# Kernel optimization log

Hardware: AMD Instinct MI355X
Metric: run time of the kernel (lower is better)

Reference implementation:

```python
import jax, jax.numpy as jnp
import numpy as np

N_QUBITS = 8
N_LAYERS = 4


def _apply_1q(state, U, q):
    """Apply a 2x2 gate U (shape (2,2) shared, or (B,2,2) per-sample) on qubit q.
    state: (B, 2, 2, ..., 2) with qubit q on axis q+1 (wire 0 = most significant)."""
    a = q + 1
    st = jnp.moveaxis(state, a, -1)
    shp = st.shape
    st = st.reshape(shp[0], -1, 2)  # (B, rest, 2)
    if U.ndim == 3:
        st = jnp.einsum('bij,brj->bri', U, st)
    else:
        st = jnp.einsum('ij,brj->bri', U, st)
    return jnp.moveaxis(st.reshape(shp), -1, a)


def _cnot(state, c, t):
    ac, at = c + 1, t + 1
    s0 = jnp.take(state, 0, axis=ac)
    s1 = jnp.take(state, 1, axis=ac)
    at2 = at - 1 if at > ac else at  # axis shift after removing control axis
    s1 = jnp.flip(s1, axis=at2)      # X on target where control = 1
    return jnp.stack([s0, s1], axis=ac)


def _rx(t):
    c = jnp.cos(t / 2)
    s = jnp.sin(t / 2)
    return jnp.stack([jnp.stack([c + 0j, -1j * s]),
                      jnp.stack([-1j * s, c + 0j])]).astype(jnp.complex64)


def _ry(t):
    c = jnp.cos(t / 2)
    s = jnp.sin(t / 2)
    return jnp.stack([jnp.stack([c, -s]),
                      jnp.stack([s, c])]).astype(jnp.complex64)


def _rz(t):
    return jnp.diag(jnp.stack([jnp.exp(-1j * t / 2),
                               jnp.exp(1j * t / 2)])).astype(jnp.complex64)


def _ry_batched(t):
    # t: (B,) -> (B, 2, 2)
    c = jnp.cos(t / 2)
    s = jnp.sin(t / 2)
    U = jnp.stack([jnp.stack([c, -s], axis=-1),
                   jnp.stack([s, c], axis=-1)], axis=-2)
    return U.astype(jnp.complex64)


def setup_inputs() -> dict:
    key = jax.random.key(0)
    k1, k2 = jax.random.split(key)
    B = 16384
    x = jax.random.normal(k1, (B, N_QUBITS), dtype=jnp.float32)
    weights = jax.random.normal(k2, (N_QUBITS * N_LAYERS * 3,), dtype=jnp.float32) * 0.1
    return {"x": x, "weights": weights}


def reference(x, weights):
    n, L = N_QUBITS, N_LAYERS
    B = x.shape[0]
    state = jnp.zeros((B,) + (2,) * n, dtype=jnp.complex64)
    state = state.at[(slice(None),) + (0,) * n].set(1.0)

    # angle encoding: per-sample RY on each wire
    for q in range(n):
        state = _apply_1q(state, _ry_batched(x[:, q]), q)

    idx = 0
    for _ in range(L):
        for q in range(n):
            state = _apply_1q(state, _rx(weights[idx]), q)
            state = _apply_1q(state, _ry(weights[idx + 1]), q)
            state = _apply_1q(state, _rz(weights[idx + 2]), q)
            idx += 3
        for q in range(n - 1):
            state = _cnot(state, q, q + 1)

    p = jnp.abs(state) ** 2  # (B, 2, ..., 2) float32
    outs = []
    for q in range(n):
        axes = tuple(a for a in range(1, n + 1) if a != q + 1)
        z = p.sum(axis=axes)  # (B, 2)
        outs.append(z[:, 0] - z[:, 1])
    return jnp.stack(outs, axis=-1).astype(jnp.float32)
```

## Files before the change

kernel.cpp:

```cpp
#include <hip/hip_runtime.h>


#define NGATES 32
typedef short s8v __attribute__((ext_vector_type(8)));
typedef float f4v __attribute__((ext_vector_type(4)));

__device__ __forceinline__ unsigned short f2bf(float f) {
    unsigned u = __float_as_uint(f);
    u += 0x7FFFu + ((u >> 16) & 1u);
    return (unsigned short)(u >> 16);
}
__device__ __forceinline__ float xsgn(float f, unsigned m) {
    return __int_as_float(__float_as_int(f) ^ (int)m);
}
template<int M>
__device__ __forceinline__ float shx(float v) {
    return __int_as_float(__builtin_amdgcn_ds_swizzle(__float_as_int(v), (M << 10) | 0x1F));
}

constexpr bool selon(int l, int d) {
    return (l == 0) ? (d == 0) : (((d + l - 1) & (l - 1)) == (l - 1));
}
constexpr int lm_of(int l, int q) {
    int m = 0;
    for (int d = 0; q + d <= 7; ++d)
        if ((l & d) == d) { int qq = q + d; if (qq <= 3) m |= 1 << (3 - qq); }
    return m;
}
constexpr int rm_of(int l, int q) {
    int m = 0;
    for (int d = 0; q + d <= 7; ++d)
        if ((l & d) == d) { int qq = q + d; if (qq >= 4) m |= 1 << (7 - qq); }
    return m;
}
constexpr int slm_of(int l, int q) {
    int m = 0;
    for (int d = 0; d <= q; ++d)
        if (selon(l, d)) { int k = q - d; if (k <= 3) m |= 1 << (3 - k); }
    return m;
}
constexpr int srm_of(int l, int q) {
    int m = 0;
    for (int d = 0; d <= q; ++d)
        if (selon(l, d)) { int k = q - d; if (k >= 4) m |= 1 << (7 - k); }
    return m;
}

template<int LM, int RM, int SLM, int SRM>
__device__ __forceinline__ void apply_gate(float ar[16], float ai[16], int lane,
                                           const float4 g)
{
    unsigned sm = 0;
    if constexpr (SLM != 0)
        sm = (unsigned)((__builtin_popcount(lane & SLM) & 1) << 31);
    const float c0r = g.x, c1i = g.w;
    const float c0i0 = xsgn(g.y, sm);
    const float c1r0 = xsgn(g.z, sm);
    const float c0i1 = xsgn(g.y, sm ^ 0x80000000u);
    const float c1r1 = xsgn(g.z, sm ^ 0x80000000u);

    if constexpr (RM == 0) {
        #pragma unroll
        for (int r = 0; r < 16; ++r) {
            const bool c1 = (__builtin_popcount(r & SRM) & 1) != 0;
            const float c0i = c1 ? c0i1 : c0i0;
            const float c1r = c1 ? c1r1 : c1r0;
            const float br = shx<LM>(ar[r]);
            const float bi = shx<LM>(ai[r]);
            const float nr = c0r*ar[r] - c0i*ai[r] + c1r*br - c1i*bi;
            const float ni = c0r*ai[r] + c0i*ar[r] + c1r*bi + c1i*br;
            ar[r] = nr; ai[r] = ni;
        }
    } else {
        #pragma unroll
        for (int r = 0; r < 16; ++r) {
            const int p = r ^ RM;
            if (p < r) continue;
            float br_r, bi_r, br_p, bi_p;
            if constexpr (LM != 0) {
                br_r = shx<LM>(ar[p]); bi_r = shx<LM>(ai[p]);
                br_p = shx<LM>(ar[r]); bi_p = shx<LM>(ai[r]);
            } else {
                br_r = ar[p]; bi_r = ai[p];
                br_p = ar[r]; bi_p = ai[r];
            }
            const bool cr = (__builtin_popcount(r & SRM) & 1) != 0;
            const bool cp = (__builtin_popcount(p & SRM) & 1) != 0;
            const float c0i_r = cr ? c0i1 : c0i0, c1r_r = cr ? c1r1 : c1r0;
            const float c0i_p = cp ? c0i1 : c0i0, c1r_p = cp ? c1r1 : c1r0;
            const float nr_r = c0r*ar[r] - c0i_r*ai[r] + c1r_r*br_r - c1i*bi_r;
            const float ni_r = c0r*ai[r] + c0i_r*ar[r] + c1r_r*bi_r + c1i*br_r;
            const float nr_p = c0r*ar[p] - c0i_p*ai[p] + c1r_p*br_p - c1i*bi_p;
            const float ni_p = c0r*ai[p] + c0i_p*ar[p] + c1r_p*bi_p + c1i*br_p;
            ar[r] = nr_r; ai[r] = ni_r;
            ar[p] = nr_p; ai[p] = ni_p;
        }
    }
}

#define GATE(L, Q) apply_gate<lm_of(L,Q), rm_of(L,Q), slm_of(L,Q), srm_of(L,Q)>( \
                       ar, ai, lane, gsh4[(L)*8+(Q)])
#define LAYER(L) GATE(L,0); GATE(L,1); GATE(L,2); GATE(L,3); \
                 GATE(L,4); GATE(L,5); GATE(L,6); GATE(L,7);

__global__ __launch_bounds__(256) void build_w(const float* __restrict__ w,
                                               unsigned short* __restrict__ W)
{
    __shared__ float4 gsh4[NGATES];
    const int tid = threadIdx.x;
    if (tid < NGATES) {
        float hx = 0.5f * w[tid*3+0];
        float hy = 0.5f * w[tid*3+1];
        float hz = 0.5f * w[tid*3+2];
        float cx = cosf(hx), sx = sinf(hx);
        float cy = cosf(hy), sy = sinf(hy);
        float cz = cosf(hz), sz = sinf(hz);
        float m00r = cy*cx,  m00i =  sy*sx;
        float m01r = -sy*cx, m01i = -cy*sx;
        gsh4[tid] = make_float4(cz*m00r + sz*m00i,
                                cz*m00i - sz*m00r,
                                cz*m01r + sz*m01i,
                                cz*m01i - sz*m01r);
    }
    __syncthreads();

    const int lane = tid & 63;
    const int il   = lane & 15;
    const int j    = blockIdx.x * 16 + (tid >> 4);

    float ar[16], ai[16];
    #pragma unroll
    for (int r = 0; r < 16; ++r) {
        ar[r] = (((j >> 4) == il) && ((j & 15) == r)) ? 1.f : 0.f;
        ai[r] = 0.f;
    }
    LAYER(0)
    LAYER(1)
    LAYER(2)
    LAYER(3)
    #pragma unroll
    for (int r = 0; r < 16; ++r) {
        const int i = (il << 4) | r;
        W[i * 256 + j]         = f2bf(ar[r]);
        W[(256 + i) * 256 + j] = f2bf(ai[r]);
    }
}

#define ELS 272

__global__ __launch_bounds__(256, 2) void gemm_z(const float* __restrict__ x,
                                                 const unsigned short* __restrict__ W,
                                                 float* __restrict__ out, int B)
{
    __shared__ __align__(16) unsigned short El[32 * ELS];
    __shared__ float zbuf[4][32][8];

    const int tid = threadIdx.x;
    const int Mbase = blockIdx.x * 32;

    #pragma unroll
    for (int ss = 0; ss < 2; ++ss) {
        const int s  = (tid >> 4) + 16 * ss;
        const int tk = tid & 15;
        const float4* xp = (const float4*)(x + (size_t)(Mbase + s) * 8);
        float4 xa = xp[0], xb = xp[1];
        float xs8[8] = {xa.x, xa.y, xa.z, xa.w, xb.x, xb.y, xb.z, xb.w};
        float c[8], sn[8];
        #pragma unroll
        for (int q = 0; q < 8; ++q) __sincosf(0.5f * xs8[q], &sn[q], &c[q]);
        float base = ((tk & 8) ? sn[0] : c[0]) * ((tk & 4) ? sn[1] : c[1])
                   * ((tk & 2) ? sn[2] : c[2]) * ((tk & 1) ? sn[3] : c[3]);
        float P45[4] = {c[4]*c[5], c[4]*sn[5], sn[4]*c[5], sn[4]*sn[5]};
        float P67[4] = {c[6]*c[7], c[6]*sn[7], sn[6]*c[7], sn[6]*sn[7]};
        unsigned short* dst = &El[s * ELS + tk * 16];
        #pragma unroll
        for (int v = 0; v < 16; ++v)
            dst[v] = f2bf(base * P45[v >> 2] * P67[v & 3]);
    }
    __syncthreads();

    const int lane = tid & 63;
    const int g    = tid >> 6;
    const int col  = lane & 15;
    const int quad = lane >> 4;
    const int nbase = g * 64;

    f4v accR[2][4], accI[2][4];
    #pragma unroll
    for (int mt = 0; mt < 2; ++mt)
        #pragma unroll
        for (int nt = 0; nt < 4; ++nt) {
            accR[mt][nt] = (f4v){0.f, 0.f, 0.f, 0.f};
            accI[mt][nt] = (f4v){0.f, 0.f, 0.f, 0.f};
        }

    const s8v* Wp = (const s8v*)W;
    const s8v* Ap = (const s8v*)El;

    s8v a0X, a1X, bRX[4], bIX[4];
    s8v a0Y, a1Y, bRY[4], bIY[4];

    a0X = Ap[col * 34 + quad];
    a1X = Ap[(16 + col) * 34 + quad];
    #pragma unroll
    for (int nt = 0; nt < 4; ++nt) {
        const int nR = nbase + nt * 16 + col;
        bRX[nt] = Wp[nR * 32 + quad];
        bIX[nt] = Wp[(nR + 256) * 32 + quad];
    }

    #pragma unroll 1
    for (int ks = 0; ks < 8; ks += 2) {
        a0Y = Ap[col * 34 + (ks + 1) * 4 + quad];
        a1Y = Ap[(16 + col) * 34 + (ks + 1) * 4 + quad];
        #pragma unroll
        for (int nt = 0; nt < 4; ++nt) {
            const int nR = nbase + nt * 16 + col;
            bRY[nt] = Wp[nR * 32 + (ks + 1) * 4 + quad];
            bIY[nt] = Wp[(nR + 256) * 32 + (ks + 1) * 4 + quad];
        }
        #pragma unroll
        for (int nt = 0; nt < 4; ++nt) {
            accR[0][nt] = __builtin_amdgcn_mfma_f32_16x16x32_bf16(a0X, bRX[nt], accR[0][nt], 0, 0, 0);
            accR[1][nt] = __builtin_amdgcn_mfma_f32_16x16x32_bf16(a1X, bRX[nt], accR[1][nt], 0, 0, 0);
            accI[0][nt] = __builtin_amdgcn_mfma_f32_16x16x32_bf16(a0X, bIX[nt], accI[0][nt], 0, 0, 0);
            accI[1][nt] = __builtin_amdgcn_mfma_f32_16x16x32_bf16(a1X, bIX[nt], accI[1][nt], 0, 0, 0);
        }
        if (ks + 2 < 8) {
            a0X = Ap[col * 34 + (ks + 2) * 4 + quad];
            a1X = Ap[(16 + col) * 34 + (ks + 2) * 4 + quad];
            #pragma unroll
            for (int nt = 0; nt < 4; ++nt) {
                const int nR = nbase + nt * 16 + col;
                bRX[nt] = Wp[nR * 32 + (ks + 2) * 4 + quad];
                bIX[nt] = Wp[(nR + 256) * 32 + (ks + 2) * 4 + quad];
            }
        }
        #pragma unroll
        for (int nt = 0; nt < 4; ++nt) {
            accR[0][nt] = __builtin_amdgcn_mfma_f32_16x16x32_bf16(a0Y, bRY[nt], accR[0][nt], 0, 0, 0);
            accR[1][nt] = __builtin_amdgcn_mfma_f32_16x16x32_bf16(a1Y, bRY[nt], accR[1][nt], 0, 0, 0);
            accI[0][nt] = __builtin_amdgcn_mfma_f32_16x16x32_bf16(a0Y, bIY[nt], accI[0][nt], 0, 0, 0);
            accI[1][nt] = __builtin_amdgcn_mfma_f32_16x16x32_bf16(a1Y, bIY[nt], accI[1][nt], 0, 0, 0);
        }
    }

    const unsigned b1 = (unsigned)(col & 1) << 31;
    const unsigned b2 = (unsigned)(col & 2) << 30;
    const unsigned b4 = (unsigned)(col & 4) << 29;
    const unsigned b8 = (unsigned)(col & 8) << 28;
    const unsigned gm1 = (unsigned)(g & 2) << 30;
    const unsigned gm0 = (unsigned)(g & 1) << 31;

    #pragma unroll
    for (int mt = 0; mt < 2; ++mt) {
        float S0[4], S1[4], S2[4];
        #pragma unroll
        for (int reg = 0; reg < 4; ++reg) {
            float p0 = accR[mt][0][reg]*accR[mt][0][reg] + accI[mt][0][reg]*accI[mt][0][reg];
            float p1 = accR[mt][1][reg]*accR[mt][1][reg] + accI[mt][1][reg]*accI[mt][1][reg];
            float p2 = accR[mt][2][reg]*accR[mt][2][reg] + accI[mt][2][reg]*accI[mt][2][reg];
            float p3 = accR[mt][3][reg]*accR[mt][3][reg] + accI[mt][3][reg]*accI[mt][3][reg];
            S0[reg] = (p0 + p1) + (p2 + p3);
            S1[reg] = (p0 + p1) - (p2 + p3);
            S2[reg] = (p0 - p1) + (p2 - p3);
        }
        #pragma unroll
        for (int reg = 0; reg < 4; ++reg) {
            float v = S0[reg];
            { float t = shx<1>(v); v = t + xsgn(v, b1); }
            { float t = shx<2>(v); v = t + xsgn(v, b2); }
            { float t = shx<4>(v); v = t + xsgn(v, b4); }
            { float t = shx<8>(v); v = t + xsgn(v, b8); }
            S0[reg] = v;
            float u = S1[reg];
            { float t = shx<1>(u); u = t + xsgn(u, b1); }
            { float t = shx<2>(u); u = t + xsgn(u, b2); }
            { float t = shx<4>(u); u = t + xsgn(u, b4); }
            { float t = shx<8>(u); u = t + xsgn(u, b8); }
            S1[reg] = u;
            float t2 = S2[reg];
            { float t = shx<1>(t2); t2 = t + xsgn(t2, b1); }
            { float t = shx<2>(t2); t2 = t + xsgn(t2, b2); }
            { float t = shx<4>(t2); t2 = t + xsgn(t2, b4); }
            { float t = shx<8>(t2); t2 = t + xsgn(t2, b8); }
            S2[reg] = t2;
        }
        #pragma unroll
        for (int reg = 0; reg < 4; ++reg) {
            const int row = mt * 16 + quad * 4 + reg;
            if (col == 0) {
                zbuf[g][row][0] = xsgn(S0[reg], gm1);
                zbuf[g][row][1] = xsgn(S0[reg], gm0);
                zbuf[g][row][2] = S1[reg];
                zbuf[g][row][3] = S2[reg];
            } else if (col == 8) {
                zbuf[g][row][4] = xsgn(S0[reg], gm1);
            } else if (col == 4) {
                zbuf[g][row][5] = xsgn(S0[reg], gm0);
            } else if (col == 2) {
                zbuf[g][row][6] = S1[reg];
            } else if (col == 1) {
                zbuf[g][row][7] = S2[reg];
            }
        }
    }
    __syncthreads();

    {
        const int row = tid >> 3, q = tid & 7;
        out[(size_t)(Mbase + row) * 8 + q] = (zbuf[0][row][q] + zbuf[1][row][q])
                                           + (zbuf[2][row][q] + zbuf[3][row][q]);
    }
}

extern "C" void kernel_launch(void* const* d_in, const int* in_sizes, int n_in,
                              void* d_out, int out_size, void* d_ws, size_t ws_size,
                              hipStream_t stream) {
    const float* x = (const float*)d_in[0];
    const float* w = (const float*)d_in[1];
    float* out = (float*)d_out;
    unsigned short* W = (unsigned short*)d_ws;
    const int B = in_sizes[0] / 8;
    build_w<<<16, 256, 0, stream>>>(w, W);
    gemm_z<<<B / 32, 256, 0, stream>>>(x, W, out, B);
}
```

Baseline: 89.73 us.

## Remap unitary-building kernel to one wavefront per column with 4 amplitudes per lane

The build_w kernel that simulates the fixed circuit on basis vectors now assigns each column to a whole 64-lane block, with each lane holding 4 amplitudes instead of 16 lanes holding 16. It launches 256 small blocks instead of 16 large ones. Qubit pairing across lanes 16-32 apart now uses __shfl_xor, and the full 2x2 gate matrix is stored so sign selection becomes a simple select. The aim is to cut per-thread serial work and register pressure in the setup kernel and spread it over more CUs, at the cost of more cross-lane shuffles and more blocks.

```diff
diff --git a/kernel.cpp b/kernel.cpp
--- a/kernel.cpp
+++ b/kernel.cpp
@@ -15,98 +15,75 @@
 }
 template<int M>
 __device__ __forceinline__ float shx(float v) {
-    return __int_as_float(__builtin_amdgcn_ds_swizzle(__float_as_int(v), (M << 10) | 0x1F));
+    if constexpr (M == 0) {
+        return v;
+    } else if constexpr (M < 32) {
+        return __int_as_float(__builtin_amdgcn_ds_swizzle(__float_as_int(v), (M << 10) | 0x1F));
+    } else {
+        return __shfl_xor(v, M, 64);
+    }
 }
 
 constexpr bool selon(int l, int d) {
     return (l == 0) ? (d == 0) : (((d + l - 1) & (l - 1)) == (l - 1));
 }
-constexpr int lm_of(int l, int q) {
+constexpr int pairmask_lane(int l, int q) {
     int m = 0;
     for (int d = 0; q + d <= 7; ++d)
-        if ((l & d) == d) { int qq = q + d; if (qq <= 3) m |= 1 << (3 - qq); }
+        if ((l & d) == d) { int qq = q + d; if (qq <= 5) m |= 1 << (5 - qq); }
     return m;
 }
-constexpr int rm_of(int l, int q) {
+constexpr int pairmask_j(int l, int q) {
     int m = 0;
     for (int d = 0; q + d <= 7; ++d)
-        if ((l & d) == d) { int qq = q + d; if (qq >= 4) m |= 1 << (7 - qq); }
+        if ((l & d) == d) { int qq = q + d; if (qq == 6) m |= 2; else if (qq == 7) m |= 1; }
     return m;
 }
-constexpr int slm_of(int l, int q) {
+constexpr int selmask_lane(int l, int q) {
     int m = 0;
     for (int d = 0; d <= q; ++d)
-        if (selon(l, d)) { int k = q - d; if (k <= 3) m |= 1 << (3 - k); }
+        if (selon(l, d)) { int k = q - d; if (k <= 5) m |= 1 << (5 - k); }
     return m;
 }
-constexpr int srm_of(int l, int q) {
+constexpr int selmask_j(int l, int q) {
     int m = 0;
     for (int d = 0; d <= q; ++d)
-        if (selon(l, d)) { int k = q - d; if (k >= 4) m |= 1 << (7 - k); }
+        if (selon(l, d)) { int k = q - d; if (k == 6) m |= 2; else if (k == 7) m |= 1; }
     return m;
 }
 
-template<int LM, int RM, int SLM, int SRM>
-__device__ __forceinline__ void apply_gate(float ar[16], float ai[16], int lane,
-                                           const float4 g)
+template<int LM, int JM, int SLM, int SJM>
+__device__ __forceinline__ void apply_gate4(float ar[4], float ai[4], int lane,
+                                            const float* __restrict__ g)
 {
-    unsigned sm = 0;
-    if constexpr (SLM != 0)
-        sm = (unsigned)((__builtin_popcount(lane & SLM) & 1) << 31);
-    const float c0r = g.x, c1i = g.w;
-    const float c0i0 = xsgn(g.y, sm);
-    const float c1r0 = xsgn(g.z, sm);
-    const float c0i1 = xsgn(g.y, sm ^ 0x80000000u);
-    const float c1r1 = xsgn(g.z, sm ^ 0x80000000u);
-
-    if constexpr (RM == 0) {
-        #pragma unroll
-        for (int r = 0; r < 16; ++r) {
-            const bool c1 = (__builtin_popcount(r & SRM) & 1) != 0;
-            const float c0i = c1 ? c0i1 : c0i0;
-            const float c1r = c1 ? c1r1 : c1r0;
-            const float br = shx<LM>(ar[r]);
-            const float bi = shx<LM>(ai[r]);
-            const float nr = c0r*ar[r] - c0i*ai[r] + c1r*br - c1i*bi;
-            const float ni = c0r*ai[r] + c0i*ar[r] + c1r*bi + c1i*br;
-            ar[r] = nr; ai[r] = ni;
-        }
-    } else {
-        #pragma unroll
-        for (int r = 0; r < 16; ++r) {
-            const int p = r ^ RM;
-            if (p < r) continue;
-            float br_r, bi_r, br_p, bi_p;
-            if constexpr (LM != 0) {
-                br_r = shx<LM>(ar[p]); bi_r = shx<LM>(ai[p]);
-                br_p = shx<LM>(ar[r]); bi_p = shx<LM>(ai[r]);
-            } else {
-                br_r = ar[p]; bi_r = ai[p];
-                br_p = ar[r]; bi_p = ai[r];
-            }
-            const bool cr = (__builtin_popcount(r & SRM) & 1) != 0;
-            const bool cp = (__builtin_popcount(p & SRM) & 1) != 0;
-            const float c0i_r = cr ? c0i1 : c0i0, c1r_r = cr ? c1r1 : c1r0;
-            const float c0i_p = cp ? c0i1 : c0i0, c1r_p = cp ? c1r1 : c1r0;
-            const float nr_r = c0r*ar[r] - c0i_r*ai[r] + c1r_r*br_r - c1i*bi_r;
-            const float ni_r = c0r*ai[r] + c0i_r*ar[r] + c1r_r*bi_r + c1i*br_r;
-            const float nr_p = c0r*ar[p] - c0i_p*ai[p] + c1r_p*br_p - c1i*bi_p;
-            const float ni_p = c0r*ai[p] + c0i_p*ar[p] + c1r_p*bi_p + c1i*br_p;
-            ar[r] = nr_r; ai[r] = ni_r;
-            ar[p] = nr_p; ai[p] = ni_p;
-        }
-    }
-}
-
-#define GATE(L, Q) apply_gate<lm_of(L,Q), rm_of(L,Q), slm_of(L,Q), srm_of(L,Q)>( \
-                       ar, ai, lane, gsh4[(L)*8+(Q)])
-#define LAYER(L) GATE(L,0); GATE(L,1); GATE(L,2); GATE(L,3); \
-                 GATE(L,4); GATE(L,5); GATE(L,6); GATE(L,7);
-
-__global__ __launch_bounds__(256) void build_w(const float* __restrict__ w,
-                                               unsigned short* __restrict__ W)
+    const bool pl = (SLM == 0) ? false : (bool)(__builtin_popcount(lane & SLM) & 1);
+    const float g0 = g[0], g1 = g[1], g2 = g[2], g3 = g[3];
+    const float g4 = g[4], g5 = g[5], g6 = g[6], g7 = g[7];
+    float nr[4], ni[4];
+    #pragma unroll
+    for (int j = 0; j < 4; ++j) {
+        const bool flip = (__builtin_popcount(j & SJM) & 1) != 0;
+        const bool s = pl != flip;
+        const float c0r = s ? g6 : g0, c0i = s ? g7 : g1;
+        const float c1r = s ? g4 : g2, c1i = s ? g5 : g3;
+        const float br = shx<LM>(ar[j ^ JM]);
+        const float bi = shx<LM>(ai[j ^ JM]);
+        nr[j] = c0r*ar[j] - c0i*ai[j] + c1r*br - c1i*bi;
+        ni[j] = c0r*ai[j] + c0i*ar[j] + c1r*bi + c1i*br;
+    }
+    #pragma unroll
+    for (int j = 0; j < 4; ++j) { ar[j] = nr[j]; ai[j] = ni[j]; }
+}
+
+#define GATE4(L, Q) apply_gate4<pairmask_lane(L,Q), pairmask_j(L,Q), \
+                                selmask_lane(L,Q), selmask_j(L,Q)>(ar, ai, lane, gsh[(L)*8+(Q)])
+#define LAYER4(L) GATE4(L,0); GATE4(L,1); GATE4(L,2); GATE4(L,3); \
+                  GATE4(L,4); GATE4(L,5); GATE4(L,6); GATE4(L,7);
+
+__global__ __launch_bounds__(64) void build_w(const float* __restrict__ w,
+                                              unsigned short* __restrict__ W)
 {
-    __shared__ float4 gsh4[NGATES];
+    __shared__ float gsh[NGATES][8];
     const int tid = threadIdx.x;
     if (tid < NGATES) {
         float hx = 0.5f * w[tid*3+0];
@@ -117,32 +94,38 @@
         float cz = cosf(hz), sz = sinf(hz);
         float m00r = cy*cx,  m00i =  sy*sx;
         float m01r = -sy*cx, m01i = -cy*sx;
-        gsh4[tid] = make_float4(cz*m00r + sz*m00i,
-                                cz*m00i - sz*m00r,
-                                cz*m01r + sz*m01i,
-                                cz*m01i - sz*m01r);
+        float m10r = sy*cx,  m10i = -cy*sx;
+        float m11r = cy*cx,  m11i = -sy*sx;
+        gsh[tid][0] = cz*m00r + sz*m00i;
+        gsh[tid][1] = cz*m00i - sz*m00r;
+        gsh[tid][2] = cz*m01r + sz*m01i;
+        gsh[tid][3] = cz*m01i - sz*m01r;
+        gsh[tid][4] = cz*m10r - sz*m10i;
+        gsh[tid][5] = cz*m10i + sz*m10r;
+        gsh[tid][6] = cz*m11r - sz*m11i;
+        gsh[tid][7] = cz*m11i + sz*m11r;
     }
     __syncthreads();
 
-    const int lane = tid & 63;
-    const int il   = lane & 15;
-    const int j    = blockIdx.x * 16 + (tid >> 4);
-
-    float ar[16], ai[16];
-    #pragma unroll
-    for (int r = 0; r < 16; ++r) {
-        ar[r] = (((j >> 4) == il) && ((j & 15) == r)) ? 1.f : 0.f;
-        ai[r] = 0.f;
-    }
-    LAYER(0)
-    LAYER(1)
-    LAYER(2)
-    LAYER(3)
-    #pragma unroll
-    for (int r = 0; r < 16; ++r) {
-        const int i = (il << 4) | r;
-        W[i * 256 + j]         = f2bf(ar[r]);
-        W[(256 + i) * 256 + j] = f2bf(ai[r]);
+    const int lane = tid;
+    const int j    = blockIdx.x;
+
+    float ar[4], ai[4];
+    #pragma unroll
+    for (int jj = 0; jj < 4; ++jj) {
+        ar[jj] = (lane == (j >> 2) && jj == (j & 3)) ? 1.f : 0.f;
+        ai[jj] = 0.f;
+    }
+    LAYER4(0)
+    LAYER4(1)
+    LAYER4(2)
+    LAYER4(3)
+
+    #pragma unroll
+    for (int jj = 0; jj < 4; ++jj) {
+        const int i = (lane << 2) | jj;
+        W[i * 256 + j]         = f2bf(ar[jj]);
+        W[(256 + i) * 256 + j] = f2bf(ai[jj]);
     }
 }
 
@@ -322,6 +305,6 @@
     float* out = (float*)d_out;
     unsigned short* W = (unsigned short*)d_ws;
     const int B = in_sizes[0] / 8;
-    build_w<<<16, 256, 0, stream>>>(w, W);
+    build_w<<<256, 64, 0, stream>>>(w, W);
     gemm_z<<<B / 32, 256, 0, stream>>>(x, W, out, B);
 }
```

After: 79.81 us. 11.1% less time.
